# Performance work log

Measured on AMD Instinct MI355X. Metric: run time of the kernel, lower is better.

## Reference

```python
import jax, jax.numpy as jnp
import numpy as np

DIM = 1024
DIM_QK = 1024
DIM_V = 1024
H = 16
SCALE = 1.0 / (DIM_QK ** 0.5)  # NOTE: module scales by sqrt(dim_qk), not sqrt(head_dim)


def setup_inputs() -> dict:
    key = jax.random.key(0)
    ks = jax.random.split(key, 12)
    B, S = 2, 2048
    q = jax.random.normal(ks[0], (B, S, DIM), jnp.float32)
    k = jax.random.normal(ks[1], (B, S, DIM), jnp.float32)
    v = jax.random.normal(ks[2], (B, S, DIM), jnp.float32)
    mask = jax.random.randint(ks[3], (B, 1, S, S), 0, 2) > 0  # True = masked
    s = 1.0 / np.sqrt(DIM)
    Wq = jax.random.uniform(ks[4], (DIM_QK, DIM), jnp.float32, -s, s)
    bq = jax.random.uniform(ks[5], (DIM_QK,), jnp.float32, -s, s)
    Wk = jax.random.uniform(ks[6], (DIM_QK, DIM), jnp.float32, -s, s)
    bk = jax.random.uniform(ks[7], (DIM_QK,), jnp.float32, -s, s)
    Wv = jax.random.uniform(ks[8], (DIM_V, DIM), jnp.float32, -s, s)
    bv = jax.random.uniform(ks[9], (DIM_V,), jnp.float32, -s, s)
    Wo = jax.random.uniform(ks[10], (DIM_V, DIM), jnp.float32, -s, s)
    bo = jax.random.uniform(ks[11], (DIM_V,), jnp.float32, -s, s)
    return {"q": q, "k": k, "v": v, "mask": mask,
            "Wq": Wq, "bq": bq, "Wk": Wk, "bk": bk,
            "Wv": Wv, "bv": bv, "Wo": Wo, "bo": bo}


def reference(q, k, v, mask, Wq, bq, Wk, bk, Wv, bv, Wo, bo):
    B, Sq, _ = q.shape
    Skv = k.shape[1]
    # projections (torch Linear: x @ W.T + b)
    qh = (q @ Wq.T + bq).reshape(B, Sq, H, DIM_QK // H).transpose(0, 2, 1, 3)   # [B,H,Sq,dk]
    kh = (k @ Wk.T + bk).reshape(B, Skv, H, DIM_QK // H).transpose(0, 2, 1, 3)  # [B,H,Skv,dk]
    vh = (v @ Wv.T + bv).reshape(B, Skv, H, DIM_V // H).transpose(0, 2, 1, 3)   # [B,H,Skv,dv]
    attn = jnp.einsum('bhqd,bhkd->bhqk', qh, kh) * SCALE
    attn = jnp.where(mask, jnp.float32(-1e20), attn)
    attn = jax.nn.softmax(attn, axis=-1)
    # dropout is identity in eval / p=0
    out = jnp.einsum('bhqk,bhkd->bhqd', attn, vh)            # [B,H,Sq,dv]
    out = out.transpose(0, 2, 1, 3).reshape(B, Sq, DIM_V)
    return out @ Wo.T + bo
```

## Files before the change

### kernel.cpp

```cpp
#include <hip/hip_runtime.h>
#include <hip/hip_bf16.h>

typedef __attribute__((ext_vector_type(8))) __bf16 bf16x8;
typedef __attribute__((ext_vector_type(4))) short short4v;
typedef __attribute__((ext_vector_type(4))) float f32x4;
typedef __attribute__((ext_vector_type(4))) unsigned int uint4v;
typedef __attribute__((ext_vector_type(2))) unsigned int uint2v;

#define S_LEN 2048
#define DIM_  1024
#define HDIM  64
#define SCALE2 0.045084441f

#define EXP2F(x) __builtin_amdgcn_exp2f(x)

#define ATTN_SWZ(row, col8) (((row) * 64) + (((col8) ^ ((row) & 7)) << 3))

__device__ __forceinline__ void async_copy16(const void* gp, void* lp) {
  __builtin_amdgcn_global_load_lds(
      (const __attribute__((address_space(1))) unsigned int*)gp,
      (__attribute__((address_space(3))) unsigned int*)lp, 16, 0, 0);
}

__device__ __forceinline__ unsigned f2bf_u(float f) {
  unsigned u = __builtin_bit_cast(unsigned, f);
  return (u + 0x7FFFu + ((u >> 16) & 1u)) >> 16;
}
__device__ __forceinline__ unsigned pack2(float a, float b) {
  return f2bf_u(a) | (f2bf_u(b) << 16);
}
__device__ __forceinline__ unsigned cvtpk(float a, float b) {
  float2 f; f.x = a; f.y = b;
  __hip_bfloat162 h = __float22bfloat162_rn(f);
  unsigned u;
  __builtin_memcpy(&u, &h, 4);
  return u;
}

__global__ __launch_bounds__(256) void cvt_kernel(
    const float* __restrict__ s0, const float* __restrict__ s1, const float* __restrict__ s2,
    const float* __restrict__ s3, const float* __restrict__ s4, const float* __restrict__ s5,
    const float* __restrict__ s6,
    __hip_bfloat16* __restrict__ d0, __hip_bfloat16* __restrict__ d1, __hip_bfloat16* __restrict__ d2,
    __hip_bfloat16* __restrict__ d3, __hip_bfloat16* __restrict__ d4, __hip_bfloat16* __restrict__ d5,
    __hip_bfloat16* __restrict__ d6,
    const int* __restrict__ mask, unsigned long long* __restrict__ bits)
{
  if (blockIdx.y == 7) {
    int wave = threadIdx.x >> 6, lane = threadIdx.x & 63;
    int gw = blockIdx.x * 4 + wave;
#pragma unroll
    for (int it = 0; it < 16; ++it) {
      int w = gw * 16 + it;
      int m = mask[(size_t)w * 64 + lane];
      unsigned long long bal = __ballot(m != 0);
      if (lane == 0) bits[w] = bal;
    }
    return;
  }
  const float* srcs[7] = {s0, s1, s2, s3, s4, s5, s6};
  __hip_bfloat16* dsts[7] = {d0, d1, d2, d3, d4, d5, d6};
  const int sizes[7] = {4194304, 4194304, 4194304, 1048576, 1048576, 1048576, 1048576};
  int rg = blockIdx.y;
  int base = (blockIdx.x * 256 + threadIdx.x) * 8;
  if (base >= sizes[rg]) return;
  const float* s = srcs[rg] + base;
  f32x4 a = *(const f32x4*)s;
  f32x4 b = *(const f32x4*)(s + 4);
  uint4v o;
  o.x = pack2(a[0], a[1]); o.y = pack2(a[2], a[3]);
  o.z = pack2(b[0], b[1]); o.w = pack2(b[2], b[3]);
  *(uint4v*)(dsts[rg] + base) = o;
}

__device__ __forceinline__ void swz(int r, int& m0, int& n0) {
  int c  = ((r & 7) << 2) | (r >> 6);
  int xl = (r >> 3) & 7;
  m0 = ((c >> 3) * 8 + xl) * 128;
  n0 = (c & 7) * 128;
}

__global__ __launch_bounds__(256) void qkv_gemm_kernel(
    const __hip_bfloat16* __restrict__ xq, const __hip_bfloat16* __restrict__ xk,
    const __hip_bfloat16* __restrict__ xv,
    const __hip_bfloat16* __restrict__ Wq, const float* __restrict__ bq,
    const __hip_bfloat16* __restrict__ Wk, const float* __restrict__ bk,
    const __hip_bfloat16* __restrict__ Wv, const float* __restrict__ bv,
    __hip_bfloat16* __restrict__ Q, __hip_bfloat16* __restrict__ Kk,
    __hip_bfloat16* __restrict__ VT)
{
  const __hip_bfloat16 *X, *W; const float* bias;
  if (blockIdx.z == 0)      { X = xq; W = Wq; bias = bq; }
  else if (blockIdx.z == 1) { X = xk; W = Wk; bias = bk; }
  else                      { X = xv; W = Wv; bias = bv; }

  constexpr int K = 1024, N = 1024;
  __shared__ alignas(16) __hip_bfloat16 SM[4][128 * 32];
  const int tid  = threadIdx.x;
  const int lane = tid & 63;
  const int wave = tid >> 6;
  const int t    = lane & 15;
  const int quad = lane >> 4;
  const int wm   = wave >> 1;
  const int wn   = wave & 1;
  int m0, n0;
  swz(blockIdx.x, m0, n0);

  f32x4 acc[4][4] = {};

  const int c0 = tid, c1 = 256 + tid;
  const int r0 = c0 >> 2, o0 = (c0 & 3) * 8;
  const int r1 = c1 >> 2, o1 = (c1 & 3) * 8;
  const __hip_bfloat16* xp0 = &X[(size_t)(m0 + r0) * K + o0];
  const __hip_bfloat16* xp1 = &X[(size_t)(m0 + r1) * K + o1];
  const __hip_bfloat16* wp0 = &W[(size_t)(n0 + r0) * K + o0];
  const __hip_bfloat16* wp1 = &W[(size_t)(n0 + r1) * K + o1];

  async_copy16(xp0, &SM[0][c0 * 8]);
  async_copy16(xp1, &SM[0][c1 * 8]);
  async_copy16(wp0, &SM[2][c0 * 8]);
  async_copy16(wp1, &SM[2][c1 * 8]);

  int buf = 0;
  for (int k0 = 0; k0 < K; k0 += 32) {
    __syncthreads();
    if (k0 + 32 < K) {
      int nb = buf ^ 1;
      int kn = k0 + 32;
      async_copy16(xp0 + kn, &SM[nb][c0 * 8]);
      async_copy16(xp1 + kn, &SM[nb][c1 * 8]);
      async_copy16(wp0 + kn, &SM[2 + nb][c0 * 8]);
      async_copy16(wp1 + kn, &SM[2 + nb][c1 * 8]);
    }
    bf16x8 a[4], b[4];
#pragma unroll
    for (int i = 0; i < 4; ++i)
      a[i] = *(const bf16x8*)&SM[buf][(wm * 64 + i * 16 + t) * 32 + quad * 8];
#pragma unroll
    for (int j = 0; j < 4; ++j)
      b[j] = *(const bf16x8*)&SM[2 + buf][(wn * 64 + j * 16 + t) * 32 + quad * 8];
#pragma unroll
    for (int i = 0; i < 4; ++i)
#pragma unroll
      for (int j = 0; j < 4; ++j)
        acc[i][j] = __builtin_amdgcn_mfma_f32_16x16x32_bf16(a[i], b[j], acc[i][j], 0, 0, 0);
    buf ^= 1;
  }

  float bj[4];
#pragma unroll
  for (int j = 0; j < 4; ++j)
    bj[j] = bias[n0 + wn * 64 + j * 16 + t];

  __syncthreads();
  __hip_bfloat16* SMf = &SM[0][0];

  if (blockIdx.z == 2) {
#pragma unroll
    for (int i = 0; i < 4; ++i) {
      int mlb = wm * 8 + i * 2 + (quad >> 1);
#pragma unroll
      for (int j = 0; j < 4; ++j) {
        int nl = wn * 64 + j * 16 + t;
        int blk = (mlb & 8) | ((mlb & 7) ^ (nl & 7));
        uint2v pk;
        pk.x = pack2(acc[i][j][0] + bj[j], acc[i][j][1] + bj[j]);
        pk.y = pack2(acc[i][j][2] + bj[j], acc[i][j][3] + bj[j]);
        *(uint2v*)&SMf[nl * 128 + blk * 8 + (quad & 1) * 4] = pk;
      }
    }
    __syncthreads();
    const int bb = m0 >> 11, kv0 = m0 & 2047;
#pragma unroll
    for (int pass = 0; pass < 8; ++pass) {
      int nl = pass * 16 + (tid >> 4);
      int lb = tid & 15;
      int blk = (lb & 8) | ((lb & 7) ^ (nl & 7));
      uint4 x = *(const uint4*)&SMf[nl * 128 + blk * 8];
      *(uint4*)&VT[(size_t)(bb * 1024 + n0 + nl) * 2048 + kv0 + lb * 8] = x;
    }
  } else {
    const bool isq = (blockIdx.z == 0);
    __hip_bfloat16* Out = isq ? Q : Kk;
    const float sc = isq ? SCALE2 : 1.0f;
#pragma unroll
    for (int i = 0; i < 4; ++i)
#pragma unroll
      for (int j = 0; j < 4; ++j) {
        int nlb = wn * 8 + j * 2 + (t >> 3);
        int nin = t & 7;
#pragma unroll
        for (int r = 0; r < 4; ++r) {
          int ml = wm * 64 + i * 16 + quad * 4 + r;
          int blk = (nlb & 8) | ((nlb & 7) ^ (ml & 7));
          SMf[ml * 128 + blk * 8 + nin] =
              __float2bfloat16((acc[i][j][r] + bj[j]) * sc);
        }
      }
    __syncthreads();
#pragma unroll
    for (int pass = 0; pass < 8; ++pass) {
      int ml = pass * 16 + (tid >> 4);
      int lb = tid & 15;
      int blk = (lb & 8) | ((lb & 7) ^ (ml & 7));
      uint4 x = *(const uint4*)&SMf[ml * 128 + blk * 8];
      *(uint4*)&Out[(size_t)(m0 + ml) * N + n0 + lb * 8] = x;
    }
  }
}

__global__ __launch_bounds__(256) void proj_gemm_kernel(
    const __hip_bfloat16* __restrict__ X, const __hip_bfloat16* __restrict__ W,
    const float* __restrict__ bias, float* __restrict__ Out)
{
  constexpr int K = 1024, N = 1024;
  __shared__ alignas(16) __hip_bfloat16 As[2][128 * 32];
  __shared__ alignas(16) __hip_bfloat16 Bs[2][128 * 32];
  const int tid  = threadIdx.x;
  const int lane = tid & 63;
  const int wave = tid >> 6;
  const int t    = lane & 15;
  const int quad = lane >> 4;
  const int wm   = wave >> 1;
  const int wn   = wave & 1;
  int m0, n0;
  swz(blockIdx.x, m0, n0);

  f32x4 acc[4][4] = {};

  const int c0 = tid, c1 = 256 + tid;
  const int r0 = c0 >> 2, o0 = (c0 & 3) * 8;
  const int r1 = c1 >> 2, o1 = (c1 & 3) * 8;
  const __hip_bfloat16* xp0 = &X[(size_t)(m0 + r0) * K + o0];
  const __hip_bfloat16* xp1 = &X[(size_t)(m0 + r1) * K + o1];
  const __hip_bfloat16* wp0 = &W[(size_t)(n0 + r0) * K + o0];
  const __hip_bfloat16* wp1 = &W[(size_t)(n0 + r1) * K + o1];

  async_copy16(xp0, &As[0][c0 * 8]);
  async_copy16(xp1, &As[0][c1 * 8]);
  async_copy16(wp0, &Bs[0][c0 * 8]);
  async_copy16(wp1, &Bs[0][c1 * 8]);

  int buf = 0;
  for (int k0 = 0; k0 < K; k0 += 32) {
    __syncthreads();
    if (k0 + 32 < K) {
      int nb = buf ^ 1;
      int kn = k0 + 32;
      async_copy16(xp0 + kn, &As[nb][c0 * 8]);
      async_copy16(xp1 + kn, &As[nb][c1 * 8]);
      async_copy16(wp0 + kn, &Bs[nb][c0 * 8]);
      async_copy16(wp1 + kn, &Bs[nb][c1 * 8]);
    }
    bf16x8 a[4], b[4];
#pragma unroll
    for (int i = 0; i < 4; ++i)
      a[i] = *(const bf16x8*)&As[buf][(wm * 64 + i * 16 + t) * 32 + quad * 8];
#pragma unroll
    for (int j = 0; j < 4; ++j)
      b[j] = *(const bf16x8*)&Bs[buf][(wn * 64 + j * 16 + t) * 32 + quad * 8];
#pragma unroll
    for (int i = 0; i < 4; ++i)
#pragma unroll
      for (int j = 0; j < 4; ++j)
        acc[i][j] = __builtin_amdgcn_mfma_f32_16x16x32_bf16(a[i], b[j], acc[i][j], 0, 0, 0);
    buf ^= 1;
  }

  float bj[4];
#pragma unroll
  for (int j = 0; j < 4; ++j)
    bj[j] = bias[n0 + wn * 64 + j * 16 + t];
#pragma unroll
  for (int i = 0; i < 4; ++i)
#pragma unroll
    for (int j = 0; j < 4; ++j)
#pragma unroll
      for (int r = 0; r < 4; ++r) {
        int m = m0 + wm * 64 + i * 16 + quad * 4 + r;
        int n = n0 + wn * 64 + j * 16 + t;
        Out[(size_t)m * N + n] = acc[i][j][r] + bj[j];
      }
}

__global__ __launch_bounds__(256) void attn_kernel(
    const __hip_bfloat16* __restrict__ Qb,
    const __hip_bfloat16* __restrict__ Kb,
    const __hip_bfloat16* __restrict__ VT,
    const unsigned long long* __restrict__ mbits,
    __hip_bfloat16* __restrict__ Ob)
{
  const int bid = blockIdx.x;
  const int qt = (bid >> 3) & 31;
  const int g  = ((bid & 7) << 2) | (bid >> 8);
  const int h  = g & 15;
  const int b  = g >> 4;
  const int qb = qt * 64;

  __shared__ alignas(16) __hip_bfloat16 Qs[64 * 64];
  __shared__ alignas(16) __hip_bfloat16 Ks[2][64 * 64];
  __shared__ alignas(16) __hip_bfloat16 Vt[2][64 * 64];

  const int tid  = threadIdx.x;
  const int lane = tid & 63;
  const int wave = tid >> 6;
  const int t    = lane & 15;
  const int quad = lane >> 4;

  const int r0 = tid >> 3;
  const int r1 = 32 + r0;
  const int k0c = ((tid & 7) ^ (r0 & 7)) << 3;
  const int k1c = ((tid & 7) ^ (r1 & 7)) << 3;
  const __hip_bfloat16* kp0 = &Kb[((size_t)(b * S_LEN + r0)) * DIM_ + h * HDIM + k0c];
  const __hip_bfloat16* kp1 = &Kb[((size_t)(b * S_LEN + r1)) * DIM_ + h * HDIM + k1c];
  const size_t vtbase = (size_t)((b * 16 + h) * 64) * 2048;
  const __hip_bfloat16* vp0 = &VT[vtbase + (size_t)r0 * 2048 + k0c];
  const __hip_bfloat16* vp1 = &VT[vtbase + (size_t)r1 * 2048 + k1c];

  async_copy16(kp0, &Ks[0][tid * 8]);
  async_copy16(kp1, &Ks[0][(256 + tid) * 8]);
  async_copy16(vp0, &Vt[0][tid * 8]);
  async_copy16(vp1, &Vt[0][(256 + tid) * 8]);

#pragma unroll
  for (int r = 0; r < 2; ++r) {
    int c = r * 256 + tid;
    int row = c >> 3, c8 = c & 7;
    uint4 raw = *(const uint4*)&Qb[((size_t)(b * S_LEN + qb + row)) * DIM_ + h * HDIM + c8 * 8];
    *(uint4*)&Qs[ATTN_SWZ(row, c8)] = raw;
  }
  __syncthreads();

  bf16x8 qf[2];
#pragma unroll
  for (int ks = 0; ks < 2; ++ks)
    qf[ks] = *(const bf16x8*)&Qs[ATTN_SWZ(wave * 16 + t, ks * 4 + quad)];

  int koff[8];
#pragma unroll
  for (int i = 0; i < 4; ++i) {
    koff[i]     = ATTN_SWZ(i * 16 + t, quad);
    koff[4 + i] = ATTN_SWZ(i * 16 + t, 4 + quad);
  }
  int voff[16];
#pragma unroll
  for (int j = 0; j < 4; ++j)
#pragma unroll
    for (int n = 0; n < 4; ++n)
      voff[j * 4 + n] = (n * 16 + t) * 64 +
          (((j * 2 + (quad >> 1)) ^ (t & 7)) << 3) + (quad & 1) * 4;

  f32x4 lp4 = {0.f, 0.f, 0.f, 0.f};
  f32x4 o[4] = {};

  const int qg = qb + wave * 16 + t;
  const size_t mbase = ((size_t)b * S_LEN + qg) * 32;
  const int qshift = quad * 4;

#define ATTN_TILE(kvt, BUF)                                                   \
  {                                                                           \
    unsigned long long mw = mbits[mbase + (kvt)];                             \
    if ((kvt) > 0) __syncthreads();                \
    if ((kvt) + 1 < 32) {                                                     \
      size_t koffg = (size_t)((kvt) + 1) * 64 * DIM_;                         \
      int    voffg = ((kvt) + 1) * 64;                                        \
      async_copy16(kp0 + koffg, &Ks[(BUF) ^ 1][tid * 8]);                     \
      async_copy16(kp1 + koffg, &Ks[(BUF) ^ 1][(256 + tid) * 8]);             \
      async_copy16(vp0 + voffg, &Vt[(BUF) ^ 1][tid * 8]);                     \
      async_copy16(vp1 + voffg, &Vt[(BUF) ^ 1][(256 + tid) * 8]);             \
    }                                                                         \
    __builtin_amdgcn_s_setprio(1);                                            \
    unsigned long long mwq = mw >> qshift;                                    \
    unsigned mlo = (unsigned)mwq, mhi = (unsigned)(mwq >> 32);                \
    unsigned mqv[4] = {mlo & 0xFu, (mlo >> 16) & 0xFu,                        \
                       mhi & 0xFu, (mhi >> 16) & 0xFu};                       \
    float e[4][4];                                                            \
    _Pragma("unroll")                                                         \
    for (int i = 0; i < 4; ++i) {                                             \
      f32x4 z = {};                                                           \
      bf16x8 a0 = *(const bf16x8*)&Ks[BUF][koff[i]];                          \
      z = __builtin_amdgcn_mfma_f32_16x16x32_bf16(a0, qf[0], z, 0, 0, 0);     \
      bf16x8 a1 = *(const bf16x8*)&Ks[BUF][koff[4 + i]];                      \
      z = __builtin_amdgcn_mfma_f32_16x16x32_bf16(a1, qf[1], z, 0, 0, 0);     \
      _Pragma("unroll")                                                       \
      for (int r = 0; r < 4; ++r) {                                           \
        float v = ((mqv[i] >> r) & 1u) ? -1e20f : z[r];                       \
        float ex = EXP2F(v);                                                  \
        e[i][r] = ex;                                                         \
        lp4[r] += ex;                                                         \
      }                                                                       \
    }                                                                         \
    short4v pf[4];                                                            \
    _Pragma("unroll")                                                         \
    for (int j = 0; j < 4; ++j) {                                             \
      uint2v pk;                                                              \
      pk.x = cvtpk(e[j][0], e[j][1]);                                         \
      pk.y = cvtpk(e[j][2], e[j][3]);                                         \
      pf[j] = __builtin_bit_cast(short4v, pk);                                \
    }                                                                         \
    _Pragma("unroll")                                                         \
    for (int j = 0; j < 4; ++j)                                               \
      _Pragma("unroll")                                                       \
      for (int n = 0; n < 4; ++n) {                                           \
        short4v va = *(const short4v*)&Vt[BUF][voff[j * 4 + n]];              \
        o[n] = __builtin_amdgcn_mfma_f32_16x16x16bf16_1k(va, pf[j], o[n],     \
                                                         0, 0, 0);            \
      }                                                                       \
    __builtin_amdgcn_s_setprio(0);                                            \
  }

  ATTN_TILE(0, 0)
  for (int kvt = 1; kvt < 31; kvt += 2) {
    ATTN_TILE(kvt, 1)
    ATTN_TILE(kvt + 1, 0)
  }
  ATTN_TILE(31, 1)
#undef ATTN_TILE

  float lp = (lp4[0] + lp4[1]) + (lp4[2] + lp4[3]);
  lp += __shfl_xor(lp, 16, 64);
  lp += __shfl_xor(lp, 32, 64);
  float rl = 1.0f / lp;

  __hip_bfloat16* Ts = Qs;
  __syncthreads();
#pragma unroll
  for (int n = 0; n < 4; ++n) {
    uint2v pk;
    pk.x = cvtpk(o[n][0] * rl, o[n][1] * rl);
    pk.y = cvtpk(o[n][2] * rl, o[n][3] * rl);
    *(uint2v*)&Ts[(wave * 16 + t) * 64 +
                  (((n * 2 + (quad >> 1)) ^ (t & 7)) << 3) + (quad & 1) * 4] = pk;
  }
  __syncthreads();
  {
    int row = tid >> 2;
    int b0  = (tid & 3) * 2;
    uint4 x0 = *(const uint4*)&Ts[row * 64 + ((b0 ^ (row & 7)) << 3)];
    uint4 x1 = *(const uint4*)&Ts[row * 64 + (((b0 + 1) ^ (row & 7)) << 3)];
    int d0 = (tid & 3) * 16;
    __hip_bfloat16* dst = &Ob[((size_t)(b * S_LEN + qb + row)) * DIM_ + h * HDIM + d0];
    *(uint4*)dst = x0;
    *(uint4*)(dst + 8) = x1;
  }
}

extern "C" void kernel_launch(void* const* d_in, const int* in_sizes, int n_in,
                              void* d_out, int out_size, void* d_ws, size_t ws_size,
                              hipStream_t stream) {
  const float* q  = (const float*)d_in[0];
  const float* k  = (const float*)d_in[1];
  const float* v  = (const float*)d_in[2];
  const int*   mk = (const int*)d_in[3];
  const float* Wq = (const float*)d_in[4];
  const float* bq = (const float*)d_in[5];
  const float* Wk = (const float*)d_in[6];
  const float* bk = (const float*)d_in[7];
  const float* Wv = (const float*)d_in[8];
  const float* bv = (const float*)d_in[9];
  const float* Wo = (const float*)d_in[10];
  const float* bo = (const float*)d_in[11];
  float* out = (float*)d_out;

  char* ws = (char*)d_ws;
  const size_t MB = 1024 * 1024;
  __hip_bfloat16* Qb  = (__hip_bfloat16*)(ws);
  __hip_bfloat16* Kb  = (__hip_bfloat16*)(ws + 8  * MB);
  __hip_bfloat16* VTb = (__hip_bfloat16*)(ws + 16 * MB);
  __hip_bfloat16* Ob  = (__hip_bfloat16*)(ws + 24 * MB);
  __hip_bfloat16* xqb = (__hip_bfloat16*)(ws + 32 * MB);
  __hip_bfloat16* xkb = (__hip_bfloat16*)(ws + 40 * MB);
  __hip_bfloat16* xvb = (__hip_bfloat16*)(ws + 48 * MB);
  __hip_bfloat16* Wqb = (__hip_bfloat16*)(ws + 56 * MB);
  __hip_bfloat16* Wkb = (__hip_bfloat16*)(ws + 58 * MB);
  __hip_bfloat16* Wvb = (__hip_bfloat16*)(ws + 60 * MB);
  __hip_bfloat16* Wob = (__hip_bfloat16*)(ws + 62 * MB);
  unsigned long long* mbits = (unsigned long long*)(ws + 64 * MB);

  cvt_kernel<<<dim3(2048, 8), 256, 0, stream>>>(q, k, v, Wq, Wk, Wv, Wo,
                                                xqb, xkb, xvb, Wqb, Wkb, Wvb, Wob,
                                                mk, mbits);
  qkv_gemm_kernel<<<dim3(256, 1, 3), 256, 0, stream>>>(xqb, xkb, xvb,
                                                       Wqb, bq, Wkb, bk, Wvb, bv,
                                                       Qb, Kb, VTb);
  attn_kernel<<<dim3(1024), 256, 0, stream>>>(Qb, Kb, VTb, mbits, Ob);
  proj_gemm_kernel<<<dim3(256), 256, 0, stream>>>(Ob, Wob, bo, out);
}
```

Measured before the change: 258.0 us.

## Switch attention kernel to 32x32x16 MFMA with two waves per block

Rewrites the attention inner loop to use 32x32x16 bf16 MFMA instructions instead of 16x16 ones, with each of two waves owning 32 query rows. The P fragment is rebuilt via cross-half lane shuffles so it can feed the PV MFMA directly. The block shrinks to 128 threads, each issuing more async loads per tile. The aim is fewer MFMA issues and LDS fragment reads per tile, at the cost of extra shuffles, higher register pressure, and fewer waves to hide latency.

New measurement: 263.0 us. No clear change (+1.9%).

```diff
diff --git a/kernel.cpp b/kernel.cpp
--- a/kernel.cpp
+++ b/kernel.cpp
@@ -4,6 +4,7 @@
 typedef __attribute__((ext_vector_type(8))) __bf16 bf16x8;
 typedef __attribute__((ext_vector_type(4))) short short4v;
 typedef __attribute__((ext_vector_type(4))) float f32x4;
+typedef __attribute__((ext_vector_type(16))) float f32x16;
 typedef __attribute__((ext_vector_type(4))) unsigned int uint4v;
 typedef __attribute__((ext_vector_type(2))) unsigned int uint2v;
 
@@ -283,7 +284,7 @@
       }
 }
 
-__global__ __launch_bounds__(256) void attn_kernel(
+__global__ __launch_bounds__(128) void attn_kernel(
     const __hip_bfloat16* __restrict__ Qb,
     const __hip_bfloat16* __restrict__ Kb,
     const __hip_bfloat16* __restrict__ VT,
@@ -304,108 +305,100 @@
   const int tid  = threadIdx.x;
   const int lane = tid & 63;
   const int wave = tid >> 6;
-  const int t    = lane & 15;
-  const int quad = lane >> 4;
-
-  const int r0 = tid >> 3;
-  const int r1 = 32 + r0;
-  const int k0c = ((tid & 7) ^ (r0 & 7)) << 3;
-  const int k1c = ((tid & 7) ^ (r1 & 7)) << 3;
-  const __hip_bfloat16* kp0 = &Kb[((size_t)(b * S_LEN + r0)) * DIM_ + h * HDIM + k0c];
-  const __hip_bfloat16* kp1 = &Kb[((size_t)(b * S_LEN + r1)) * DIM_ + h * HDIM + k1c];
+  const int qc   = lane & 31;
+  const int hh   = lane >> 5;
+
+  const int srow = tid >> 3;
+  const int scol = ((tid & 7) ^ (srow & 7)) << 3;
+  const __hip_bfloat16* kpp = &Kb[((size_t)(b * S_LEN + srow)) * DIM_ + h * HDIM + scol];
   const size_t vtbase = (size_t)((b * 16 + h) * 64) * 2048;
-  const __hip_bfloat16* vp0 = &VT[vtbase + (size_t)r0 * 2048 + k0c];
-  const __hip_bfloat16* vp1 = &VT[vtbase + (size_t)r1 * 2048 + k1c];
-
-  async_copy16(kp0, &Ks[0][tid * 8]);
-  async_copy16(kp1, &Ks[0][(256 + tid) * 8]);
-  async_copy16(vp0, &Vt[0][tid * 8]);
-  async_copy16(vp1, &Vt[0][(256 + tid) * 8]);
-
-#pragma unroll
-  for (int r = 0; r < 2; ++r) {
-    int c = r * 256 + tid;
+  const __hip_bfloat16* vpp = &VT[vtbase + (size_t)srow * 2048 + scol];
+
+#pragma unroll
+  for (int i = 0; i < 4; ++i) {
+    async_copy16(kpp + (size_t)i * 16 * DIM_, &Ks[0][(i * 128 + tid) * 8]);
+    async_copy16(vpp + (size_t)i * 16 * 2048, &Vt[0][(i * 128 + tid) * 8]);
+  }
+
+#pragma unroll
+  for (int i = 0; i < 4; ++i) {
+    int c = i * 128 + tid;
     int row = c >> 3, c8 = c & 7;
     uint4 raw = *(const uint4*)&Qb[((size_t)(b * S_LEN + qb + row)) * DIM_ + h * HDIM + c8 * 8];
     *(uint4*)&Qs[ATTN_SWZ(row, c8)] = raw;
   }
   __syncthreads();
 
-  bf16x8 qf[2];
-#pragma unroll
-  for (int ks = 0; ks < 2; ++ks)
-    qf[ks] = *(const bf16x8*)&Qs[ATTN_SWZ(wave * 16 + t, ks * 4 + quad)];
-
-  int koff[8];
-#pragma unroll
-  for (int i = 0; i < 4; ++i) {
-    koff[i]     = ATTN_SWZ(i * 16 + t, quad);
-    koff[4 + i] = ATTN_SWZ(i * 16 + t, 4 + quad);
-  }
-  int voff[16];
+  bf16x8 qf[4];
 #pragma unroll
   for (int j = 0; j < 4; ++j)
-#pragma unroll
-    for (int n = 0; n < 4; ++n)
-      voff[j * 4 + n] = (n * 16 + t) * 64 +
-          (((j * 2 + (quad >> 1)) ^ (t & 7)) << 3) + (quad & 1) * 4;
+    qf[j] = *(const bf16x8*)&Qs[ATTN_SWZ(wave * 32 + qc, 2 * j + hh)];
 
   f32x4 lp4 = {0.f, 0.f, 0.f, 0.f};
-  f32x4 o[4] = {};
-
-  const int qg = qb + wave * 16 + t;
-  const size_t mbase = ((size_t)b * S_LEN + qg) * 32;
-  const int qshift = quad * 4;
+  f32x16 oacc[2] = {};
+
+  const size_t mbase = ((size_t)b * S_LEN + qb + wave * 32 + qc) * 32;
 
 #define ATTN_TILE(kvt, BUF)                                                   \
   {                                                                           \
     unsigned long long mw = mbits[mbase + (kvt)];                             \
-    if ((kvt) > 0) __syncthreads();                \
+    if ((kvt) > 0) __syncthreads();                                           \
     if ((kvt) + 1 < 32) {                                                     \
-      size_t koffg = (size_t)((kvt) + 1) * 64 * DIM_;                         \
-      int    voffg = ((kvt) + 1) * 64;                                        \
-      async_copy16(kp0 + koffg, &Ks[(BUF) ^ 1][tid * 8]);                     \
-      async_copy16(kp1 + koffg, &Ks[(BUF) ^ 1][(256 + tid) * 8]);             \
-      async_copy16(vp0 + voffg, &Vt[(BUF) ^ 1][tid * 8]);                     \
-      async_copy16(vp1 + voffg, &Vt[(BUF) ^ 1][(256 + tid) * 8]);             \
+      size_t ko = (size_t)((kvt) + 1) * 64 * DIM_;                            \
+      int    vo = ((kvt) + 1) * 64;                                           \
+      _Pragma("unroll")                                                       \
+      for (int i = 0; i < 4; ++i) {                                           \
+        async_copy16(kpp + ko + (size_t)i * 16 * DIM_,                        \
+                     &Ks[(BUF) ^ 1][(i * 128 + tid) * 8]);                    \
+        async_copy16(vpp + vo + (size_t)i * 16 * 2048,                        \
+                     &Vt[(BUF) ^ 1][(i * 128 + tid) * 8]);                    \
+      }                                                                       \
     }                                                                         \
     __builtin_amdgcn_s_setprio(1);                                            \
-    unsigned long long mwq = mw >> qshift;                                    \
-    unsigned mlo = (unsigned)mwq, mhi = (unsigned)(mwq >> 32);                \
-    unsigned mqv[4] = {mlo & 0xFu, (mlo >> 16) & 0xFu,                        \
-                       mhi & 0xFu, (mhi >> 16) & 0xFu};                       \
-    float e[4][4];                                                            \
     _Pragma("unroll")                                                         \
-    for (int i = 0; i < 4; ++i) {                                             \
-      f32x4 z = {};                                                           \
-      bf16x8 a0 = *(const bf16x8*)&Ks[BUF][koff[i]];                          \
-      z = __builtin_amdgcn_mfma_f32_16x16x32_bf16(a0, qf[0], z, 0, 0, 0);     \
-      bf16x8 a1 = *(const bf16x8*)&Ks[BUF][koff[4 + i]];                      \
-      z = __builtin_amdgcn_mfma_f32_16x16x32_bf16(a1, qf[1], z, 0, 0, 0);     \
+    for (int T = 0; T < 2; ++T) {                                             \
+      f32x16 z = {};                                                          \
       _Pragma("unroll")                                                       \
-      for (int r = 0; r < 4; ++r) {                                           \
-        float v = ((mqv[i] >> r) & 1u) ? -1e20f : z[r];                       \
-        float ex = EXP2F(v);                                                  \
-        e[i][r] = ex;                                                         \
-        lp4[r] += ex;                                                         \
+      for (int j = 0; j < 4; ++j) {                                           \
+        bf16x8 kf = *(const bf16x8*)&Ks[BUF][ATTN_SWZ(T * 32 + qc, 2 * j + hh)];\
+        z = __builtin_amdgcn_mfma_f32_32x32x16_bf16(kf, qf[j], z, 0, 0, 0);   \
+      }                                                                       \
+      unsigned u = (unsigned)(mw >> (T * 32 + 4 * hh));                       \
+      unsigned Dm[4][2];                                                      \
+      _Pragma("unroll")                                                       \
+      for (int m = 0; m < 4; ++m) {                                           \
+        unsigned nib = (u >> (8 * m)) & 0xFu;                                 \
+        float e0 = EXP2F((nib & 1u) ? -1e20f : z[4 * m + 0]);                 \
+        float e1 = EXP2F((nib & 2u) ? -1e20f : z[4 * m + 1]);                 \
+        float e2 = EXP2F((nib & 4u) ? -1e20f : z[4 * m + 2]);                 \
+        float e3 = EXP2F((nib & 8u) ? -1e20f : z[4 * m + 3]);                 \
+        lp4[0] += e0; lp4[1] += e1; lp4[2] += e2; lp4[3] += e3;               \
+        Dm[m][0] = cvtpk(e0, e1);                                             \
+        Dm[m][1] = cvtpk(e2, e3);                                             \
+      }                                                                       \
+      _Pragma("unroll")                                                       \
+      for (int ks = 0; ks < 2; ++ks) {                                        \
+        unsigned A0 = Dm[2 * ks][0],     A1 = Dm[2 * ks][1];                  \
+        unsigned B0 = Dm[2 * ks + 1][0], B1 = Dm[2 * ks + 1][1];              \
+        unsigned pA0 = __shfl_xor(A0, 32, 64);                                \
+        unsigned pA1 = __shfl_xor(A1, 32, 64);                                \
+        unsigned pB0 = __shfl_xor(B0, 32, 64);                                \
+        unsigned pB1 = __shfl_xor(B1, 32, 64);                                \
+        uint4v wv;                                                            \
+        wv.x = hh ? pB0 : A0;                                                 \
+        wv.y = hh ? pB1 : A1;                                                 \
+        wv.z = hh ? B0 : pA0;                                                 \
+        wv.w = hh ? B1 : pA1;                                                 \
+        bf16x8 pfrag = __builtin_bit_cast(bf16x8, wv);                        \
+        _Pragma("unroll")                                                     \
+        for (int G = 0; G < 2; ++G) {                                         \
+          bf16x8 vfrag = *(const bf16x8*)&Vt[BUF][                            \
+              ATTN_SWZ(G * 32 + qc, 4 * T + 2 * ks + hh)];                    \
+          oacc[G] = __builtin_amdgcn_mfma_f32_32x32x16_bf16(vfrag, pfrag,     \
+                                                            oacc[G], 0, 0, 0);\
+        }                                                                     \
       }                                                                       \
     }                                                                         \
-    short4v pf[4];                                                            \
-    _Pragma("unroll")                                                         \
-    for (int j = 0; j < 4; ++j) {                                             \
-      uint2v pk;                                                              \
-      pk.x = cvtpk(e[j][0], e[j][1]);                                         \
-      pk.y = cvtpk(e[j][2], e[j][3]);                                         \
-      pf[j] = __builtin_bit_cast(short4v, pk);                                \
-    }                                                                         \
-    _Pragma("unroll")                                                         \
-    for (int j = 0; j < 4; ++j)                                               \
-      _Pragma("unroll")                                                       \
-      for (int n = 0; n < 4; ++n) {                                           \
-        short4v va = *(const short4v*)&Vt[BUF][voff[j * 4 + n]];              \
-        o[n] = __builtin_amdgcn_mfma_f32_16x16x16bf16_1k(va, pf[j], o[n],     \
-                                                         0, 0, 0);            \
-      }                                                                       \
     __builtin_amdgcn_s_setprio(0);                                            \
   }
 
@@ -418,30 +411,39 @@
 #undef ATTN_TILE
 
   float lp = (lp4[0] + lp4[1]) + (lp4[2] + lp4[3]);
-  lp += __shfl_xor(lp, 16, 64);
   lp += __shfl_xor(lp, 32, 64);
   float rl = 1.0f / lp;
 
   __hip_bfloat16* Ts = Qs;
   __syncthreads();
-#pragma unroll
-  for (int n = 0; n < 4; ++n) {
-    uint2v pk;
-    pk.x = cvtpk(o[n][0] * rl, o[n][1] * rl);
-    pk.y = cvtpk(o[n][2] * rl, o[n][3] * rl);
-    *(uint2v*)&Ts[(wave * 16 + t) * 64 +
-                  (((n * 2 + (quad >> 1)) ^ (t & 7)) << 3) + (quad & 1) * 4] = pk;
+  {
+    int row = wave * 32 + qc;
+#pragma unroll
+    for (int G = 0; G < 2; ++G)
+#pragma unroll
+      for (int m = 0; m < 4; ++m) {
+        uint2v pk;
+        pk.x = cvtpk(oacc[G][4 * m + 0] * rl, oacc[G][4 * m + 1] * rl);
+        pk.y = cvtpk(oacc[G][4 * m + 2] * rl, oacc[G][4 * m + 3] * rl);
+        *(uint2v*)&Ts[row * 64 + (((4 * G + m) ^ (row & 7)) << 3) + 4 * hh] = pk;
+      }
   }
   __syncthreads();
   {
-    int row = tid >> 2;
-    int b0  = (tid & 3) * 2;
-    uint4 x0 = *(const uint4*)&Ts[row * 64 + ((b0 ^ (row & 7)) << 3)];
-    uint4 x1 = *(const uint4*)&Ts[row * 64 + (((b0 + 1) ^ (row & 7)) << 3)];
-    int d0 = (tid & 3) * 16;
-    __hip_bfloat16* dst = &Ob[((size_t)(b * S_LEN + qb + row)) * DIM_ + h * HDIM + d0];
-    *(uint4*)dst = x0;
-    *(uint4*)(dst + 8) = x1;
+#pragma unroll
+    for (int i = 0; i < 2; ++i) {
+      int tt = i * 128 + tid;
+      int row = tt >> 2;
+      int half = (tt >> 1) & 1;
+      int bb = tt & 1;
+      __hip_bfloat16* dst = &Ob[((size_t)(b * S_LEN + qb + row)) * DIM_ + h * HDIM];
+#pragma unroll
+      for (int s = 0; s < 2; ++s) {
+        int blk = half * 4 + bb * 2 + s;
+        uint4 x = *(const uint4*)&Ts[row * 64 + ((blk ^ (row & 7)) << 3)];
+        *(uint4*)(dst + blk * 8) = x;
+      }
+    }
   }
 }
 
@@ -483,6 +485,6 @@
   qkv_gemm_kernel<<<dim3(256, 1, 3), 256, 0, stream>>>(xqb, xkb, xvb,
                                                        Wqb, bq, Wkb, bk, Wvb, bv,
                                                        Qb, Kb, VTb);
-  attn_kernel<<<dim3(1024), 256, 0, stream>>>(Qb, Kb, VTb, mbits, Ob);
+  attn_kernel<<<dim3(1024), 128, 0, stream>>>(Qb, Kb, VTb, mbits, Ob);
   proj_gemm_kernel<<<dim3(256), 256, 0, stream>>>(Ob, Wob, bo, out);
 }
```
